# Kernel tuning notes

Hardware: AMD Instinct MI355X
Metric: run time of the kernel (lower is better)

The kernel has to match this reference:

```python
import jax, jax.numpy as jnp
import numpy as np

B, S, D, H = 2, 2048, 1024, 16
HD = D // H  # head_dim = 64


def setup_inputs() -> dict:
    key = jax.random.key(0)
    ks = jax.random.split(key, 5)
    scale = 0.02
    return {
        "x": jax.random.normal(ks[0], (B, S, D), dtype=jnp.float32),
        "w_qkv": jax.random.normal(ks[1], (D, 3 * D), dtype=jnp.float32) * scale,
        "b_qkv": jax.random.normal(ks[2], (3 * D,), dtype=jnp.float32) * scale,
        "w_out": jax.random.normal(ks[3], (D, D), dtype=jnp.float32) * scale,
        "b_out": jax.random.normal(ks[4], (D,), dtype=jnp.float32) * scale,
    }


def reference(x, w_qkv, b_qkv, w_out, b_out):
    b, s, d = x.shape
    qkv = x @ w_qkv + b_qkv                       # [b,s,3d]
    q, k, v = jnp.split(qkv, 3, axis=-1)
    # split heads -> [b,h,s,hd]
    def split_heads(t):
        return t.reshape(b, s, H, HD).transpose(0, 2, 1, 3)
    q, k, v = split_heads(q), split_heads(k), split_heads(v)
    scores = jnp.einsum('bhqd,bhkd->bhqk', q, k) / jnp.sqrt(jnp.float32(HD))
    causal = jnp.tril(jnp.ones((s, s), dtype=bool))  # [s,s]
    scores = jnp.where(causal[None, None], scores, -jnp.inf)
    attn = jax.nn.softmax(scores, axis=-1)        # dropout_p=0 -> identity
    ctx = jnp.einsum('bhqk,bhkd->bhqd', attn, v)
    ctx = ctx.transpose(0, 2, 1, 3).reshape(b, s, d)  # merge heads
    return ctx @ w_out + b_out
```

## Files before the change

kernel.cpp:

```cpp
#include <hip/hip_runtime.h>
#include <hip/hip_bf16.h>

#define B_ 2
#define S_ 2048
#define D_ 1024
#define H_ 16
#define HD_ 64
#define KDIM 1024
#define QKVW 3072

typedef __attribute__((ext_vector_type(8))) short s16x8;
typedef __attribute__((ext_vector_type(8))) __bf16 bf16x8;
typedef __attribute__((ext_vector_type(4))) float f32x4;
typedef __attribute__((ext_vector_type(16))) float f32x16;
typedef __attribute__((ext_vector_type(4))) unsigned short u16x4;

__device__ __forceinline__ unsigned short f2bf(float f) {
  union { __bf16 b; unsigned short u; } v;
  v.b = (__bf16)f;
  return v.u;
}

__device__ __forceinline__ unsigned pk2(float lo, float hi) {
  union { unsigned short s[2]; unsigned u; } r;
  r.s[0] = f2bf(lo); r.s[1] = f2bf(hi);
  return r.u;
}

__device__ __forceinline__ void plswap2(unsigned& a_out, unsigned& b_out,
                                        unsigned a, unsigned b) {
  auto rr = __builtin_amdgcn_permlane32_swap(a, b, false, false);
  unsigned out[2];
  __builtin_memcpy(out, &rr, 8);
  a_out = out[0];
  b_out = out[1];
}

#define MFMA16(a, b, c) __builtin_amdgcn_mfma_f32_16x16x32_bf16((a), (b), (c), 0, 0, 0)
#define MFMA32(a, b, c) __builtin_amdgcn_mfma_f32_32x32x16_bf16((a), (b), (c), 0, 0, 0)

__device__ __forceinline__ void gll16(const void* g, void* l) {
  __builtin_amdgcn_global_load_lds(
      (const __attribute__((address_space(1))) void*)g,
      (__attribute__((address_space(3))) void*)l, 16, 0, 0);
}

__global__ __launch_bounds__(256) void prep(const float* __restrict__ X,
                                            unsigned short* __restrict__ Xb,
                                            const float* __restrict__ Wq,
                                            unsigned short* __restrict__ WqT,
                                            const float* __restrict__ Wo,
                                            unsigned short* __restrict__ WoT) {
  const int bid = blockIdx.x;
  const int t = threadIdx.x;
  if (bid < 2048) {
    const int i = (bid * 256 + t) * 8;
    const float4 a = *reinterpret_cast<const float4*>(X + i);
    const float4 b = *reinterpret_cast<const float4*>(X + i + 4);
    u16x4 lo = {f2bf(a.x), f2bf(a.y), f2bf(a.z), f2bf(a.w)};
    u16x4 hi = {f2bf(b.x), f2bf(b.y), f2bf(b.z), f2bf(b.w)};
    *reinterpret_cast<u16x4*>(Xb + i) = lo;
    *reinterpret_cast<u16x4*>(Xb + i + 4) = hi;
    return;
  }
  __shared__ float T[64][65];
  const float* W;
  unsigned short* Wt;
  int N, k0, n0;
  if (bid < 2048 + 768) {
    const int i = bid - 2048;
    W = Wq; Wt = WqT; N = 3072;
    n0 = (i % 48) * 64; k0 = (i / 48) * 64;
  } else {
    const int i = bid - 2816;
    W = Wo; Wt = WoT; N = 1024;
    n0 = (i % 16) * 64; k0 = (i / 16) * 64;
  }
  const int lr = t >> 4, lc = (t & 15) * 4;
#pragma unroll
  for (int p = 0; p < 4; ++p) {
    const int r = lr + p * 16;
    const float4 v = *reinterpret_cast<const float4*>(W + (size_t)(k0 + r) * N + n0 + lc);
    T[r][lc + 0] = v.x; T[r][lc + 1] = v.y; T[r][lc + 2] = v.z; T[r][lc + 3] = v.w;
  }
  __syncthreads();
  const int wn = t >> 4, wk = (t & 15) * 4;
#pragma unroll
  for (int p = 0; p < 4; ++p) {
    const int n = wn + p * 16;
    u16x4 o = {f2bf(T[wk + 0][n]), f2bf(T[wk + 1][n]), f2bf(T[wk + 2][n]), f2bf(T[wk + 3][n])};
    *reinterpret_cast<u16x4*>(Wt + (size_t)(n0 + n) * 1024 + k0 + wk) = o;
  }
}

__global__ __launch_bounds__(256) void vtrans(const unsigned short* __restrict__ QKVc,
                                              unsigned short* __restrict__ Vt) {
  __shared__ unsigned short T[64][72];
  const int s0 = blockIdx.x * 64;
  const int bh = blockIdx.y;
  const int bb = bh >> 4, hh = bh & 15;
  const int t = threadIdx.x;
  const size_t base = (size_t)bh * (S_ * HD_);
  const int r = t >> 3, c8 = (t & 7) * 8;
#pragma unroll
  for (int p = 0; p < 2; ++p)
    *reinterpret_cast<s16x8*>(&T[r + p * 32][c8]) =
        *reinterpret_cast<const s16x8*>(
            QKVc + (size_t)(bb * S_ + s0 + r + p * 32) * QKVW + 2048 + hh * 64 + c8);
  __syncthreads();
  const int hd = t & 63, sg = (t >> 6) * 8;
#pragma unroll
  for (int p = 0; p < 2; ++p) {
    unsigned short tmp[8];
#pragma unroll
    for (int j = 0; j < 8; ++j) tmp[j] = T[sg + p * 32 + j][hd];
    *reinterpret_cast<s16x8*>(Vt + base + (size_t)hd * S_ + s0 + sg + p * 32) =
        *reinterpret_cast<s16x8*>(tmp);
  }
}

__global__ __launch_bounds__(256) void gemm_qkv(
    const unsigned short* __restrict__ Xb, const unsigned short* __restrict__ WT,
    const float* __restrict__ bias, unsigned short* __restrict__ Cq) {
  __shared__ __align__(16) unsigned short As[128 * 64];
  __shared__ __align__(16) unsigned short Bs[128 * 64];
  const int bid = blockIdx.y * 24 + blockIdx.x;
  const int wg = (bid & 7) * 96 + (bid >> 3);
  const int n0 = (wg % 24) * 128, m0 = (wg / 24) * 128;
  const int t = threadIdx.x;
  const int lane = t & 63, wid = t >> 6;
  const int wr = wid >> 1, wc = wid & 1;
  const int l15 = lane & 15, l16 = lane >> 4;
  const int srow = lane >> 3, scol = ((lane & 7) ^ srow) << 3;
  f32x4 acc[4][4] = {};
  for (int k0 = 0; k0 < KDIM; k0 += 64) {
#pragma unroll
    for (int c = 0; c < 4; ++c) {
      const int r8 = wid * 32 + c * 8;
      gll16(Xb + (size_t)(m0 + r8 + srow) * KDIM + k0 + scol, &As[r8 * 64]);
      gll16(WT + (size_t)(n0 + r8 + srow) * KDIM + k0 + scol, &Bs[r8 * 64]);
    }
    __syncthreads();
    const int key = (l15 & 7) << 4;
    const char* ab = (const char*)As + (wr * 64 + l15) * 128;
    const char* bb = (const char*)Bs + (wc * 64 + l15) * 128;
#pragma unroll
    for (int ks = 0; ks < 2; ++ks) {
      bf16x8 af[4], bfr[4];
#pragma unroll
      for (int m = 0; m < 4; ++m)
        af[m] = *(const bf16x8*)(ab + m * 2048 + ((ks * 64 + l16 * 16) ^ key));
#pragma unroll
      for (int n = 0; n < 4; ++n)
        bfr[n] = *(const bf16x8*)(bb + n * 2048 + ((ks * 64 + l16 * 16) ^ key));
#pragma unroll
      for (int m = 0; m < 4; ++m)
#pragma unroll
        for (int n = 0; n < 4; ++n)
          acc[m][n] = MFMA16(af[m], bfr[n], acc[m][n]);
    }
    __syncthreads();
  }
#pragma unroll
  for (int n = 0; n < 4; ++n) {
    const int col = n0 + wc * 64 + n * 16 + l15;
    const float bv = bias[col];
#pragma unroll
    for (int m = 0; m < 4; ++m) {
#pragma unroll
      for (int j = 0; j < 4; ++j) {
        const int row = m0 + wr * 64 + m * 16 + l16 * 4 + j;
        Cq[(size_t)row * QKVW + col] = f2bf(acc[m][n][j] + bv);
      }
    }
  }
}

__global__ __launch_bounds__(256, 3) void attn(
    const unsigned short* __restrict__ QKVc, const unsigned short* __restrict__ Vt,
    unsigned short* __restrict__ Cxt) {
  __shared__ __align__(16) unsigned short Kl[2][2][4096];
  __shared__ __align__(16) unsigned short Vl[2][4096];
  const int bi = blockIdx.x;
  const int xcd = bi & 7, slot = bi >> 3;
  const int bh = xcd * 4 + (slot & 3);
  const int qt = 31 - (slot >> 2);
  const int t = threadIdx.x, lane = t & 63, wid = t >> 6;
  const int qw = wid & 1, pw = wid >> 1;
  const int l31 = lane & 31, h = lane >> 5;
  const int h8 = h * 8, h16 = h * 16, h4 = h * 4;
  const int bb = bh >> 4, hh = bh & 15;
  const size_t base = (size_t)bh * (S_ * HD_);
  const int q0 = qt * 64 + qw * 32;
  const float NEG = -1e30f;
  const float SCALE = 0.18033688011112042f;
  const float FM = 10.0f;
  const int srow = lane >> 3;
  const int scol = ((lane & 7) ^ srow) << 3;

  bf16x8 qf[4];
  {
    const unsigned short* qp =
        QKVc + (size_t)(bb * S_ + q0 + l31) * QKVW + hh * 64 + h8;
#pragma unroll
    for (int ks = 0; ks < 4; ++ks) qf[ks] = *reinterpret_cast<const bf16x8*>(qp + ks * 16);
  }
  f32x16 o0 = {}, o1 = {};
  float lacc[8] = {};

#define STAGEK(buf, kvb)                                                              \
  do {                                                                                \
    _Pragma("unroll") for (int c = 0; c < 8; ++c)                                     \
      gll16(QKVc + (size_t)(bb * S_ + (kvb) + c * 8 + srow) * QKVW + 1024 +           \
                hh * 64 + scol,                                                       \
            &Kl[buf][pw][c * 8 * 64]);                                                \
  } while (0)

#define STAGEV(kvb)                                                                   \
  do {                                                                                \
    _Pragma("unroll") for (int c = 0; c < 8; ++c)                                     \
      gll16(Vt + base + (size_t)(c * 8 + srow) * S_ + (kvb) + scol,                   \
            &Vl[pw][c * 8 * 64]);                                                     \
  } while (0)

#define COMPUTE_QK(cb, tcur)                                                         \
  do {                                                                               \
    const int kv0 = (tcur) * 64;                                                     \
    const bool diag = (kv0 + 63 > q0);                                               \
    const char* kbase = (const char*)&Kl[cb][pw][0];                                 \
    const int key = (l31 & 7) << 4;                                                  \
    f32x16 s0 = {}, s1 = {};                                                         \
    __builtin_amdgcn_s_setprio(1);                                                   \
    _Pragma("unroll") for (int ks = 0; ks < 4; ++ks) {                               \
      bf16x8 ka = *(const bf16x8*)(kbase + l31 * 128 + ((ks * 32 + h16) ^ key));     \
      s0 = MFMA32(ka, qf[ks], s0);                                                   \
    }                                                                                \
    if (f2) {                                                                        \
      _Pragma("unroll") for (int ks = 0; ks < 4; ++ks) {                             \
        bf16x8 kb = *(const bf16x8*)(kbase + (32 + l31) * 128 + ((ks * 32 + h16) ^ key)); \
        s1 = MFMA32(kb, qf[ks], s1);                                                 \
      }                                                                              \
    }                                                                                \
    __builtin_amdgcn_s_setprio(0);                                                   \
    if (diag) {                                                                      \
      const int lim0 = q0 + l31 - kv0;                                               \
      const int lim1 = lim0 - 32;                                                    \
      _Pragma("unroll") for (int r = 0; r < 16; ++r) {                               \
        const int cr = (r & 3) + 8 * (r >> 2) + h4;                                  \
        if (cr > lim0) s0[r] = NEG;                                                  \
        if (f2 && cr > lim1) s1[r] = NEG;                                            \
      }                                                                              \
    }                                                                                \
    _Pragma("unroll") for (int r = 0; r < 16; ++r)                                   \
      s0[r] = exp2f(fmaf(s0[r], SCALE, -FM));                                        \
    if (f2) {                                                                        \
      _Pragma("unroll") for (int r = 0; r < 16; ++r)                                 \
        s1[r] = exp2f(fmaf(s1[r], SCALE, -FM));                                      \
    }                                                                                \
    _Pragma("unroll") for (int r = 0; r < 8; ++r) {                                  \
      float ps = s0[r] + s0[r + 8];                                                  \
      if (f2) ps += s1[r] + s1[r + 8];                                               \
      lacc[r] += ps;                                                                 \
    }                                                                                \
    {                                                                                \
      union { unsigned u[4]; bf16x8 v; } uu;                                         \
      unsigned a0, a1, a2, a3, w0, w1, w2, w3;                                       \
      w0 = pk2(s0[0], s0[1]); w1 = pk2(s0[2], s0[3]);                                \
      w2 = pk2(s0[4], s0[5]); w3 = pk2(s0[6], s0[7]);                                \
      plswap2(a0, a2, w0, w2); plswap2(a1, a3, w1, w3);                              \
      uu.u[0] = a0; uu.u[1] = a1; uu.u[2] = a2; uu.u[3] = a3; pa[0] = uu.v;          \
      w0 = pk2(s0[8], s0[9]); w1 = pk2(s0[10], s0[11]);                              \
      w2 = pk2(s0[12], s0[13]); w3 = pk2(s0[14], s0[15]);                            \
      plswap2(a0, a2, w0, w2); plswap2(a1, a3, w1, w3);                              \
      uu.u[0] = a0; uu.u[1] = a1; uu.u[2] = a2; uu.u[3] = a3; pa[1] = uu.v;          \
      if (f2) {                                                                      \
        w0 = pk2(s1[0], s1[1]); w1 = pk2(s1[2], s1[3]);                              \
        w2 = pk2(s1[4], s1[5]); w3 = pk2(s1[6], s1[7]);                              \
        plswap2(a0, a2, w0, w2); plswap2(a1, a3, w1, w3);                            \
        uu.u[0] = a0; uu.u[1] = a1; uu.u[2] = a2; uu.u[3] = a3; pa[2] = uu.v;        \
        w0 = pk2(s1[8], s1[9]); w1 = pk2(s1[10], s1[11]);                            \
        w2 = pk2(s1[12], s1[13]); w3 = pk2(s1[14], s1[15]);                          \
        plswap2(a0, a2, w0, w2); plswap2(a1, a3, w1, w3);                            \
        uu.u[0] = a0; uu.u[1] = a1; uu.u[2] = a2; uu.u[3] = a3; pa[3] = uu.v;        \
      }                                                                              \
    }                                                                                \
  } while (0)

#define COMPUTE_PV()                                                                 \
  do {                                                                               \
    const char* vbase = (const char*)&Vl[pw][0];                                     \
    const int key = (l31 & 7) << 4;                                                  \
    __builtin_amdgcn_s_setprio(1);                                                   \
    _Pragma("unroll") for (int hb = 0; hb < 2; ++hb) {                               \
      _Pragma("unroll") for (int ks = 0; ks < 4; ++ks)                               \
        if (f2 || ks < 2) {                                                          \
          bf16x8 va = *(const bf16x8*)(vbase + (hb * 32 + l31) * 128 +               \
                                       ((ks * 32 + h16) ^ key));                     \
          if (hb == 0) o0 = MFMA32(va, pa[ks], o0);                                  \
          else         o1 = MFMA32(va, pa[ks], o1);                                  \
        }                                                                            \
    }                                                                                \
    __builtin_amdgcn_s_setprio(0);                                                   \
  } while (0)

  const int npair = (qt >> 1) + 1;
  if (qw == 0 && pw <= qt) STAGEK(0, pw * 64);
  for (int p = 0; p < npair; ++p) {
    const int cb = p & 1;
    const int tcur = 2 * p + pw;
    if (qw == 1 && tcur <= qt) STAGEV(tcur * 64);
    if (qw == 0) {
      if (tcur + 2 <= qt) {
        STAGEK(cb ^ 1, (tcur + 2) * 64);
        __asm__ volatile("s_waitcnt vmcnt(8)" ::: "memory");
      } else {
        __asm__ volatile("s_waitcnt vmcnt(0)" ::: "memory");
      }
    }
    __builtin_amdgcn_s_barrier();
    bf16x8 pa[4];
    const bool f2 = (tcur * 64 + 32 <= q0 + 31);
    if (tcur <= qt) COMPUTE_QK(cb, tcur);
    if (qw == 1) __asm__ volatile("s_waitcnt vmcnt(0)" ::: "memory");
    __builtin_amdgcn_s_barrier();
    if (tcur <= qt) COMPUTE_PV();
    __builtin_amdgcn_s_barrier();
  }

  float lrow = 0.f;
#pragma unroll
  for (int r = 0; r < 8; ++r) lrow += lacc[r];
  lrow += __shfl_xor(lrow, 32);

  float* mb = (float*)&Kl[0][0][0];
  const int mi = qw * 2112 + lane * 33;
  if (pw == 1) {
#pragma unroll
    for (int r = 0; r < 16; ++r) { mb[mi + r] = o0[r]; mb[mi + 16 + r] = o1[r]; }
    mb[mi + 32] = lrow;
  }
  __syncthreads();
  if (pw == 1) return;
#pragma unroll
  for (int r = 0; r < 16; ++r) { o0[r] += mb[mi + r]; o1[r] += mb[mi + 16 + r]; }
  lrow += mb[mi + 32];

  float* obuf = (float*)&Vl[0][0] + (size_t)qw * 2048;
  const float rl = 1.0f / lrow;
#pragma unroll
  for (int r = 0; r < 16; ++r) {
    const int cr = (r & 3) + 8 * (r >> 2) + h4;
    obuf[l31 * 64 + (cr ^ ((l31 & 7) << 2))] = o0[r] * rl;
    obuf[l31 * 64 + ((32 + cr) ^ ((l31 & 7) << 2))] = o1[r] * rl;
  }
  __asm__ volatile("s_waitcnt lgkmcnt(0)" ::: "memory");
#pragma unroll
  for (int p = 0; p < 8; ++p) {
    const int r = (lane >> 4) + p * 4;
    const int ce = ((lane & 15) * 4) ^ ((r & 7) << 2);
    const f32x4 v = *reinterpret_cast<const f32x4*>(&obuf[r * 64 + ce]);
    u16x4 wv = {f2bf(v[0]), f2bf(v[1]), f2bf(v[2]), f2bf(v[3])};
    *reinterpret_cast<u16x4*>(&Cxt[base + (size_t)(q0 + r) * HD_ + (lane & 15) * 4]) = wv;
  }
}

__global__ __launch_bounds__(256) void gemm_out(
    const unsigned short* __restrict__ Cxt, const unsigned short* __restrict__ WT,
    const float* __restrict__ bias, float* __restrict__ out) {
  constexpr int NM = 1024;
  __shared__ __align__(16) unsigned short As[128 * 64];
  __shared__ __align__(16) unsigned short Bs[128 * 64];
  const int bid = blockIdx.y * 8 + blockIdx.x;
  const int wg = (bid & 7) * 32 + (bid >> 3);
  const int n0 = (wg % 8) * 128, m0 = (wg / 8) * 128;
  const int t = threadIdx.x;
  const int lane = t & 63, wid = t >> 6;
  const int wr = wid >> 1, wc = wid & 1;
  const int l15 = lane & 15, l16 = lane >> 4;
  const int srow = lane >> 3, scol = ((lane & 7) ^ srow) << 3;
  f32x4 acc[4][4] = {};
  for (int k0 = 0; k0 < KDIM; k0 += 64) {
    const int head = k0 >> 6;
#pragma unroll
    for (int c = 0; c < 4; ++c) {
      const int r8 = wid * 32 + c * 8;
      const int gr = m0 + r8 + srow;
      const unsigned short* asrc =
          Cxt + ((((size_t)(gr >> 11) * H_ + head) << 11) + (gr & 2047)) * HD_ + scol;
      gll16(asrc, &As[r8 * 64]);
      gll16(WT + (size_t)(n0 + r8 + srow) * KDIM + k0 + scol, &Bs[r8 * 64]);
    }
    __syncthreads();
    const int key = (l15 & 7) << 4;
    const char* ab = (const char*)As + (wr * 64 + l15) * 128;
    const char* bb = (const char*)Bs + (wc * 64 + l15) * 128;
#pragma unroll
    for (int ks = 0; ks < 2; ++ks) {
      bf16x8 af[4], bfr[4];
#pragma unroll
      for (int m = 0; m < 4; ++m)
        af[m] = *(const bf16x8*)(ab + m * 2048 + ((ks * 64 + l16 * 16) ^ key));
#pragma unroll
      for (int n = 0; n < 4; ++n)
        bfr[n] = *(const bf16x8*)(bb + n * 2048 + ((ks * 64 + l16 * 16) ^ key));
#pragma unroll
      for (int m = 0; m < 4; ++m)
#pragma unroll
        for (int n = 0; n < 4; ++n)
          acc[m][n] = MFMA16(af[m], bfr[n], acc[m][n]);
    }
    __syncthreads();
  }
#pragma unroll
  for (int n = 0; n < 4; ++n) {
    const int col = n0 + wc * 64 + n * 16 + l15;
    const float bv = bias[col];
#pragma unroll
    for (int m = 0; m < 4; ++m) {
#pragma unroll
      for (int j = 0; j < 4; ++j) {
        const int row = m0 + wr * 64 + m * 16 + l16 * 4 + j;
        out[(size_t)row * NM + col] = acc[m][n][j] + bv;
      }
    }
  }
}

extern "C" void kernel_launch(void* const* d_in, const int* in_sizes, int n_in,
                              void* d_out, int out_size, void* d_ws, size_t ws_size,
                              hipStream_t stream) {
  const float* x = (const float*)d_in[0];
  const float* w_qkv = (const float*)d_in[1];
  const float* b_qkv = (const float*)d_in[2];
  const float* w_out = (const float*)d_in[3];
  const float* b_out = (const float*)d_in[4];
  float* out = (float*)d_out;

  const size_t NTOK = (size_t)B_ * H_ * S_ * HD_;
  unsigned short* QKVc = (unsigned short*)d_ws;
  unsigned short* Vt = QKVc + (size_t)4096 * QKVW;
  unsigned short* WqT = Vt + NTOK;
  unsigned short* WoT = WqT + (size_t)3072 * 1024;
  unsigned short* Xbf = WoT + (size_t)1024 * 1024;
  unsigned short* Cxt = Xbf;

  hipLaunchKernelGGL(prep, dim3(2048 + 768 + 256), dim3(256), 0, stream,
                     x, Xbf, w_qkv, WqT, w_out, WoT);
  hipLaunchKernelGGL(gemm_qkv, dim3(24, 32), dim3(256), 0, stream, Xbf, WqT, b_qkv, QKVc);
  hipLaunchKernelGGL(vtrans, dim3(32, 32), dim3(256), 0, stream, QKVc, Vt);
  hipLaunchKernelGGL(attn, dim3(1024), dim3(256), 0, stream, QKVc, Vt, Cxt);
  hipLaunchKernelGGL(gemm_out, dim3(8, 32), dim3(256), 0, stream, Cxt, WoT, b_out, out);
}
```

Before: 124.3 us.

## Double-buffer LDS tiles in QKV and output GEMMs with XCD-aware tile mapping

Both projection GEMMs now use two LDS buffers. The next K tile's global-to-LDS loads are issued before computing on the current tile, with explicit vmcnt waits and raw barriers, so memory latency overlaps MFMA work. The block-to-tile mapping is also changed so each XCD covers a compact rectangle of M and N tiles, which should improve L2 reuse. The cost is doubled LDS per block (64 KB), which may reduce occupancy, and reliance on hand-counted vmcnt values being correct.

```diff
diff --git a/kernel.cpp b/kernel.cpp
--- a/kernel.cpp
+++ b/kernel.cpp
@@ -122,28 +122,41 @@
 __global__ __launch_bounds__(256) void gemm_qkv(
     const unsigned short* __restrict__ Xb, const unsigned short* __restrict__ WT,
     const float* __restrict__ bias, unsigned short* __restrict__ Cq) {
-  __shared__ __align__(16) unsigned short As[128 * 64];
-  __shared__ __align__(16) unsigned short Bs[128 * 64];
+  __shared__ __align__(16) unsigned short As[2][128 * 64];
+  __shared__ __align__(16) unsigned short Bs[2][128 * 64];
   const int bid = blockIdx.y * 24 + blockIdx.x;
-  const int wg = (bid & 7) * 96 + (bid >> 3);
-  const int n0 = (wg % 24) * 128, m0 = (wg / 24) * 128;
+  const int xcd = bid & 7, rr = bid >> 3;
+  const int m0 = ((xcd >> 1) * 8 + (rr & 7)) * 128;
+  const int n0 = ((xcd & 1) * 12 + (rr >> 3)) * 128;
   const int t = threadIdx.x;
   const int lane = t & 63, wid = t >> 6;
   const int wr = wid >> 1, wc = wid & 1;
   const int l15 = lane & 15, l16 = lane >> 4;
   const int srow = lane >> 3, scol = ((lane & 7) ^ srow) << 3;
   f32x4 acc[4][4] = {};
-  for (int k0 = 0; k0 < KDIM; k0 += 64) {
-#pragma unroll
-    for (int c = 0; c < 4; ++c) {
-      const int r8 = wid * 32 + c * 8;
-      gll16(Xb + (size_t)(m0 + r8 + srow) * KDIM + k0 + scol, &As[r8 * 64]);
-      gll16(WT + (size_t)(n0 + r8 + srow) * KDIM + k0 + scol, &Bs[r8 * 64]);
-    }
-    __syncthreads();
+
+#define GSTAGE(buf, k0)                                                              \
+  do {                                                                               \
+    _Pragma("unroll") for (int c = 0; c < 4; ++c) {                                  \
+      const int r8 = wid * 32 + c * 8;                                               \
+      gll16(Xb + (size_t)(m0 + r8 + srow) * KDIM + (k0) + scol, &As[buf][r8 * 64]);  \
+      gll16(WT + (size_t)(n0 + r8 + srow) * KDIM + (k0) + scol, &Bs[buf][r8 * 64]);  \
+    }                                                                                \
+  } while (0)
+
+  GSTAGE(0, 0);
+  for (int kt = 0; kt < 16; ++kt) {
+    const int cur = kt & 1;
+    if (kt + 1 < 16) {
+      GSTAGE(cur ^ 1, (kt + 1) * 64);
+      __asm__ volatile("s_waitcnt vmcnt(8)" ::: "memory");
+    } else {
+      __asm__ volatile("s_waitcnt vmcnt(0)" ::: "memory");
+    }
+    __builtin_amdgcn_s_barrier();
     const int key = (l15 & 7) << 4;
-    const char* ab = (const char*)As + (wr * 64 + l15) * 128;
-    const char* bb = (const char*)Bs + (wc * 64 + l15) * 128;
+    const char* ab = (const char*)&As[cur][0] + (wr * 64 + l15) * 128;
+    const char* bb = (const char*)&Bs[cur][0] + (wc * 64 + l15) * 128;
 #pragma unroll
     for (int ks = 0; ks < 2; ++ks) {
       bf16x8 af[4], bfr[4];
@@ -159,7 +172,7 @@
         for (int n = 0; n < 4; ++n)
           acc[m][n] = MFMA16(af[m], bfr[n], acc[m][n]);
     }
-    __syncthreads();
+    __builtin_amdgcn_s_barrier();
   }
 #pragma unroll
   for (int n = 0; n < 4; ++n) {
@@ -368,32 +381,44 @@
     const unsigned short* __restrict__ Cxt, const unsigned short* __restrict__ WT,
     const float* __restrict__ bias, float* __restrict__ out) {
   constexpr int NM = 1024;
-  __shared__ __align__(16) unsigned short As[128 * 64];
-  __shared__ __align__(16) unsigned short Bs[128 * 64];
+  __shared__ __align__(16) unsigned short As[2][128 * 64];
+  __shared__ __align__(16) unsigned short Bs[2][128 * 64];
   const int bid = blockIdx.y * 8 + blockIdx.x;
-  const int wg = (bid & 7) * 32 + (bid >> 3);
-  const int n0 = (wg % 8) * 128, m0 = (wg / 8) * 128;
+  const int xcd = bid & 7, rr = bid >> 3;
+  const int m0 = ((xcd >> 1) * 8 + (rr & 7)) * 128;
+  const int n0 = ((xcd & 1) * 4 + (rr >> 3)) * 128;
   const int t = threadIdx.x;
   const int lane = t & 63, wid = t >> 6;
   const int wr = wid >> 1, wc = wid & 1;
   const int l15 = lane & 15, l16 = lane >> 4;
   const int srow = lane >> 3, scol = ((lane & 7) ^ srow) << 3;
   f32x4 acc[4][4] = {};
-  for (int k0 = 0; k0 < KDIM; k0 += 64) {
-    const int head = k0 >> 6;
-#pragma unroll
-    for (int c = 0; c < 4; ++c) {
-      const int r8 = wid * 32 + c * 8;
-      const int gr = m0 + r8 + srow;
-      const unsigned short* asrc =
-          Cxt + ((((size_t)(gr >> 11) * H_ + head) << 11) + (gr & 2047)) * HD_ + scol;
-      gll16(asrc, &As[r8 * 64]);
-      gll16(WT + (size_t)(n0 + r8 + srow) * KDIM + k0 + scol, &Bs[r8 * 64]);
-    }
-    __syncthreads();
+
+#define OSTAGE(buf, k0)                                                              \
+  do {                                                                               \
+    const int head = (k0) >> 6;                                                      \
+    _Pragma("unroll") for (int c = 0; c < 4; ++c) {                                  \
+      const int r8 = wid * 32 + c * 8;                                               \
+      const int gr = m0 + r8 + srow;                                                 \
+      gll16(Cxt + ((((size_t)(gr >> 11) * H_ + head) << 11) + (gr & 2047)) * HD_ + scol, \
+            &As[buf][r8 * 64]);                                                      \
+      gll16(WT + (size_t)(n0 + r8 + srow) * KDIM + (k0) + scol, &Bs[buf][r8 * 64]);  \
+    }                                                                                \
+  } while (0)
+
+  OSTAGE(0, 0);
+  for (int kt = 0; kt < 16; ++kt) {
+    const int cur = kt & 1;
+    if (kt + 1 < 16) {
+      OSTAGE(cur ^ 1, (kt + 1) * 64);
+      __asm__ volatile("s_waitcnt vmcnt(8)" ::: "memory");
+    } else {
+      __asm__ volatile("s_waitcnt vmcnt(0)" ::: "memory");
+    }
+    __builtin_amdgcn_s_barrier();
     const int key = (l15 & 7) << 4;
-    const char* ab = (const char*)As + (wr * 64 + l15) * 128;
-    const char* bb = (const char*)Bs + (wc * 64 + l15) * 128;
+    const char* ab = (const char*)&As[cur][0] + (wr * 64 + l15) * 128;
+    const char* bb = (const char*)&Bs[cur][0] + (wc * 64 + l15) * 128;
 #pragma unroll
     for (int ks = 0; ks < 2; ++ks) {
       bf16x8 af[4], bfr[4];
@@ -409,7 +434,7 @@
         for (int n = 0; n < 4; ++n)
           acc[m][n] = MFMA16(af[m], bfr[n], acc[m][n]);
     }
-    __syncthreads();
+    __builtin_amdgcn_s_barrier();
   }
 #pragma unroll
   for (int n = 0; n < 4; ++n) {
```

New measurement: 119.6 us. -3.8%, faster.
